# Kernel optimization log

Hardware: AMD Instinct MI355X
Metric: run time of the kernel (lower is better)

## Reference

```python
import jax, jax.numpy as jnp
import numpy as np

B, T, C, H = 4, 2048, 1024, 16
D = C // H  # head_dim = 64


def setup_inputs() -> dict:
    key = jax.random.key(0)
    ks = jax.random.split(key, 4)
    scale = 1.0 / np.sqrt(C)
    return {
        "x": jax.random.normal(ks[0], (B, T, C), dtype=jnp.float32),
        "attn_mask": jnp.ones((B, T), dtype=jnp.int32),
        "W_qkv": jax.random.normal(ks[1], (C, 3 * C), dtype=jnp.float32) * scale,
        "b_qkv": jnp.zeros((3 * C,), dtype=jnp.float32),
        "W_proj": jax.random.normal(ks[2], (C, C), dtype=jnp.float32) * scale,
        "b_proj": jnp.zeros((C,), dtype=jnp.float32),
    }


def reference(x, attn_mask, W_qkv, b_qkv, W_proj, b_proj):
    b, t, c = x.shape
    qkv = x @ W_qkv + b_qkv                      # (B,T,3C)
    q, k, v = jnp.split(qkv, 3, axis=-1)
    # b t (h d) -> b h t d
    q = q.reshape(b, t, H, D).transpose(0, 2, 1, 3)
    k = k.reshape(b, t, H, D).transpose(0, 2, 1, 3)
    v = v.reshape(b, t, H, D).transpose(0, 2, 1, 3)
    att = jnp.einsum("bhtd,bhsd->bhts", q, k) / jnp.sqrt(jnp.float32(D))
    causal = jnp.tril(jnp.ones((t, t), dtype=bool))[None, None]       # (1,1,T,T)
    pad = (attn_mask[:, None, None, :t] != 0)                         # (B,1,1,T)
    att = jnp.where(causal & pad, att, -jnp.inf)
    att = jax.nn.softmax(att, axis=-1)
    y = jnp.einsum("bhts,bhsd->bhtd", att, v)   # (B,H,T,D)
    y = y.transpose(0, 2, 1, 3).reshape(b, t, c)
    return y @ W_proj + b_proj
```

## Files before the change

### kernel.cpp

```cpp
#include <hip/hip_runtime.h>
#include <math.h>

#define B_ 4
#define T_ 2048
#define C_ 1024
#define H_ 16
#define D_ 64
#define M_ (B_*T_)
#define N1_ (3*C_)

typedef __attribute__((ext_vector_type(8))) short bf16x8;
typedef __attribute__((ext_vector_type(4))) short bf16x4;
typedef __attribute__((ext_vector_type(4))) float f32x4;
typedef __attribute__((ext_vector_type(16))) float f32x16;

__device__ __forceinline__ short f2bf(float f){
  union { float f; unsigned u; } v; v.f = f;
  unsigned r = (v.u + 0x7fffu + ((v.u >> 16) & 1u)) >> 16;
  return (short)r;
}

__device__ __forceinline__ unsigned cvtpk(float lo, float hi){
  unsigned r;
  asm("v_cvt_pk_bf16_f32 %0, %1, %2" : "=v"(r) : "v"(lo), "v"(hi));
  return r;
}

__device__ __forceinline__ void plswap(unsigned &a, unsigned &b){
  asm volatile("v_permlane32_swap_b32 %0, %1" : "+v"(a), "+v"(b));
}
__device__ __forceinline__ float xhalf_add(float x){
  unsigned a = __float_as_uint(x), b = a;
  asm volatile("v_permlane32_swap_b32 %0, %1" : "+v"(a), "+v"(b));
  return __uint_as_float(a) + __uint_as_float(b);
}

__device__ __forceinline__ void gll16(const void* g, void* l){
  __builtin_amdgcn_global_load_lds((const __attribute__((address_space(1))) void*)g,
                                   (__attribute__((address_space(3))) void*)l, 16, 0, 0);
}

__global__ __launch_bounds__(256) void convx(const float* __restrict__ x, short* __restrict__ xb, int n){
  int i = (blockIdx.x*256 + threadIdx.x)*8;
  if (i >= n) return;
  float4 a = *(const float4*)(x+i), b = *(const float4*)(x+i+4);
  bf16x8 o;
  o[0]=f2bf(a.x); o[1]=f2bf(a.y); o[2]=f2bf(a.z); o[3]=f2bf(a.w);
  o[4]=f2bf(b.x); o[5]=f2bf(b.y); o[6]=f2bf(b.z); o[7]=f2bf(b.w);
  *(bf16x8*)(xb+i) = o;
}

__global__ __launch_bounds__(256) void transw(const float* __restrict__ W, short* __restrict__ Wt, int K, int N){
  __shared__ float tl[64][72];
  int tid = threadIdx.x;
  int n0 = blockIdx.x*64, k0 = blockIdx.y*64;
  #pragma unroll
  for (int i=0;i<4;i++){
    int row = (tid>>4) + i*16;
    int col4 = (tid&15)*4;
    float4 v = *(const float4*)&W[(size_t)(k0+row)*N + n0 + col4];
    *(float4*)&tl[row][col4] = v;
  }
  __syncthreads();
  #pragma unroll
  for (int i=0;i<2;i++){
    int nr = (tid>>3) + i*32;
    int ch = tid&7;
    bf16x8 o;
    #pragma unroll
    for (int e=0;e<8;e++) o[e] = f2bf(tl[ch*8+e][nr]);
    *(bf16x8*)&Wt[(size_t)(n0+nr)*K + k0 + ch*8] = o;
  }
}

template<int OUTBF>
__global__ __launch_bounds__(256) void gemm_bt(const short* __restrict__ A, const short* __restrict__ Bt,
           const float* __restrict__ bias, short* __restrict__ outb, float* __restrict__ outf,
           int M, int N, int K)
{
  __shared__ short As[128*32];
  __shared__ short Bs[128*32];
  const int tid = threadIdx.x;
  const int wv = tid >> 6, ln = tid & 63;
  const int lnr = ln & 15, lg = ln >> 4;
  const int nx = gridDim.x;
  const int nwg = nx * gridDim.y;
  const int lin = blockIdx.x + nx * blockIdx.y;
  const int swz = (lin & 7) * (nwg >> 3) + (lin >> 3);
  const int m0 = (swz / nx) * 128, n0 = (swz % nx) * 128;
  const int wm = wv >> 1, wn = wv & 1;

  int aoff[4], boff[4];
  #pragma unroll
  for (int mi=0;mi<4;mi++){
    int row = wm*64 + mi*16 + lnr;
    aoff[mi] = row*64 + ((lg ^ ((row>>1)&3)) << 4);
  }
  #pragma unroll
  for (int ni=0;ni<4;ni++){
    int row = wn*64 + ni*16 + lnr;
    boff[ni] = row*64 + ((lg ^ ((row>>1)&3)) << 4);
  }

  f32x4 acc[4][4];
  #pragma unroll
  for(int i=0;i<4;i++)
    #pragma unroll
    for(int j=0;j<4;j++) acc[i][j] = (f32x4){0.f,0.f,0.f,0.f};

  for (int k0 = 0; k0 < K; k0 += 32){
    #pragma unroll
    for (int c = 0; c < 2; c++){
      int i = c*256 + tid;
      int r = i >> 2;
      int blk = (i&3) ^ ((r>>1)&3);
      gll16(A  + (size_t)(m0 + r)*K + k0 + blk*8, (void*)(As + (c*256 + wv*64)*8));
      gll16(Bt + (size_t)(n0 + r)*K + k0 + blk*8, (void*)(Bs + (c*256 + wv*64)*8));
    }
    __syncthreads();
    bf16x8 af[4], bfr[4];
    #pragma unroll
    for (int mi=0;mi<4;mi++) af[mi]  = *(const bf16x8*)((const char*)As + aoff[mi]);
    #pragma unroll
    for (int ni=0;ni<4;ni++) bfr[ni] = *(const bf16x8*)((const char*)Bs + boff[ni]);
    #pragma unroll
    for (int mi=0;mi<4;mi++)
      #pragma unroll
      for (int ni=0;ni<4;ni++)
        acc[mi][ni] = __builtin_amdgcn_mfma_f32_16x16x32_bf16(af[mi], bfr[ni], acc[mi][ni], 0,0,0);
    __syncthreads();
  }

  #pragma unroll
  for (int mi=0;mi<4;mi++){
    #pragma unroll
    for (int ni=0;ni<4;ni++){
      int col = n0 + wn*64 + ni*16 + lnr;
      float bv = bias[col];
      #pragma unroll
      for (int r=0;r<4;r++){
        int row = m0 + wm*64 + mi*16 + lg*4 + r;
        float v = acc[mi][ni][r] + bv;
        if (OUTBF) outb[(size_t)row*N + col] = f2bf(v);
        else       outf[(size_t)row*N + col] = v;
      }
    }
  }
}

__global__ __launch_bounds__(256) void transv(const short* __restrict__ qkv, short* __restrict__ vt){
  __shared__ short tl[64][72];
  int tid = threadIdx.x;
  int t0 = blockIdx.x*64, bh = blockIdx.y;
  int b = bh>>4, h = bh&15;
  int tr = tid>>2, cc = (tid&3)*16;
  const short* src = &qkv[(size_t)(b*T_ + t0 + tr)*N1_ + 2*C_ + h*D_ + cc];
  #pragma unroll
  for (int i=0;i<4;i++){
    bf16x4 v = *(const bf16x4*)(src + i*4);
    *(bf16x4*)&tl[tr][cc + i*4] = v;
  }
  __syncthreads();
  int d = tid>>2, tc = (tid&3)*16;
  #pragma unroll
  for (int i=0;i<2;i++){
    bf16x8 o;
    #pragma unroll
    for (int e=0;e<8;e++) o[e] = tl[tc + i*8 + e][d];
    *(bf16x8*)&vt[(size_t)(bh*D_ + d)*T_ + t0 + tc + i*8] = o;
  }
}

__global__ __launch_bounds__(256) void attn9(const short* __restrict__ qkv, const short* __restrict__ vt,
           const int* __restrict__ mask, short* __restrict__ yb)
{
  __shared__ short Ks[2][64*64];
  __shared__ short Vs[2][64*64];
  const int tid = threadIdx.x;
  const int wv = tid>>6, ln = tid&63;
  const int l31 = ln & 31, hi = ln >> 5;
  const int bh = blockIdx.x, b = bh>>4, hd = bh&15;
  const int c = 15 - (int)blockIdx.y;
  const float cexp = 0.18033688f;
  const float MC   = 11.541561f;

  const int srow = tid>>3;
  const int scol = (tid&7) ^ (srow&7);
  const short* kgb = qkv + (size_t)(b*T_ + srow)*N1_ + C_ + hd*D_ + scol*8;
  const short* vgb = vt  + (size_t)((bh<<6) + srow)*T_ + scol*8;
  int fa[4];
  #pragma unroll
  for (int i=0;i<4;i++)
    fa[i] = l31*128 + ((((i<<1)+hi) ^ (l31&7)) << 4);

  const int q0w = c*128 + wv*32;
  const int ntb  = 2*c + 2;
  const int myNt = 2*c + 1 + (wv>>1);

  bf16x8 qf[4];
  const short* qbase = qkv + (size_t)(b*T_ + q0w + l31)*N1_ + hd*D_ + hi*8;
  #pragma unroll
  for (int ds=0; ds<4; ds++) qf[ds] = *(const bf16x8*)(qbase + ds*16);

  f32x16 o0, o1;
  #pragma unroll
  for (int r=0;r<16;r++){ o0[r]=0.f; o1[r]=0.f; }
  float lsum = 0.f;

  int mv_next = mask[b*T_ + ln];
  {
    char* kd = (char*)Ks[0]; char* vd = (char*)Vs[0];
    gll16(kgb,                  kd + wv*1024);
    gll16(kgb + (size_t)32*N1_, kd + 4096 + wv*1024);
    gll16(vgb,                  vd + wv*1024);
    gll16(vgb + (size_t)32*T_,  vd + 4096 + wv*1024);
  }
  __syncthreads();

  #pragma unroll 1
  for (int jt = 0; jt < ntb; jt++){
    const int j0 = jt << 6;
    int mv_cur = mv_next;
    if (jt+1 < ntb){
      mv_next = mask[b*T_ + ((jt+1)<<6) + ln];
      char* kd = (char*)Ks[(jt+1)&1]; char* vd = (char*)Vs[(jt+1)&1];
      const short* kg = kgb + (size_t)((jt+1)<<6)*N1_;
      const short* vg = vgb + ((jt+1)<<6);
      gll16(kg,                  kd + wv*1024);
      gll16(kg + (size_t)32*N1_, kd + 4096 + wv*1024);
      gll16(vg,                  vd + wv*1024);
      gll16(vg + (size_t)32*T_,  vd + 4096 + wv*1024);
    }
    unsigned long long bm = __ballot(mv_cur != 0);

    if (jt < myNt){
      const char* ksb = (const char*)Ks[jt&1];
      const char* vsb = (const char*)Vs[jt&1];
      f32x16 s0, s1;
      #pragma unroll
      for (int r=0;r<16;r++){ s0[r]=0.f; s1[r]=0.f; }
      __builtin_amdgcn_s_setprio(1);
      #pragma unroll
      for (int ds=0; ds<4; ds++){
        bf16x8 k0 = *(const bf16x8*)(ksb + fa[ds]);
        bf16x8 k1 = *(const bf16x8*)(ksb + fa[ds] + 4096);
        s0 = __builtin_amdgcn_mfma_f32_32x32x16_bf16(k0, qf[ds], s0, 0,0,0);
        s1 = __builtin_amdgcn_mfma_f32_32x32x16_bf16(k1, qf[ds], s1, 0,0,0);
      }
      __builtin_amdgcn_s_setprio(0);

      const int qglob = q0w + l31;
      const bool allm = (bm == ~0ull);
      if (!allm){
        #pragma unroll
        for (int r=0;r<16;r++){
          int kr = (r&3) + 8*(r>>2) + 4*hi;
          bool ok0 = (j0 + kr      <= qglob) && ((bm >> kr) & 1);
          bool ok1 = (j0 + kr + 32 <= qglob) && ((bm >> (kr+32)) & 1);
          s0[r] = ok0 ? s0[r] : -INFINITY;
          s1[r] = ok1 ? s1[r] : -INFINITY;
        }
      } else if (j0 + 63 > q0w){
        #pragma unroll
        for (int r=0;r<16;r++){
          int kr = (r&3) + 8*(r>>2) + 4*hi;
          s0[r] = (j0 + kr      <= qglob) ? s0[r] : -INFINITY;
          s1[r] = (j0 + kr + 32 <= qglob) ? s1[r] : -INFINITY;
        }
      }

      #pragma unroll
      for (int r=0;r<16;r++){
        s0[r] = __builtin_amdgcn_exp2f(__builtin_fmaf(s0[r], cexp, -MC));
        s1[r] = __builtin_amdgcn_exp2f(__builtin_fmaf(s1[r], cexp, -MC));
      }
      float u[8];
      #pragma unroll
      for (int i=0;i<8;i++) u[i] = (s0[i]+s0[i+8]) + (s1[i]+s1[i+8]);
      #pragma unroll
      for (int i=0;i<4;i++) u[i] = u[i] + u[i+4];
      float ps = (u[0]+u[1]) + (u[2]+u[3]);
      lsum += xhalf_add(ps);

      unsigned LA[2][4], LB[2][4];
      #pragma unroll
      for (int rq=0; rq<4; rq++){
        LA[0][rq] = cvtpk(s0[4*rq],   s0[4*rq+1]);
        LB[0][rq] = cvtpk(s0[4*rq+2], s0[4*rq+3]);
        LA[1][rq] = cvtpk(s1[4*rq],   s1[4*rq+1]);
        LB[1][rq] = cvtpk(s1[4*rq+2], s1[4*rq+3]);
      }

      #pragma unroll
      for (int kt2=0; kt2<4; kt2++){
        const int kt = kt2>>1, sub = kt2&1;
        bf16x8 v0 = *(const bf16x8*)(vsb + fa[kt2]);
        bf16x8 v1 = *(const bf16x8*)(vsb + fa[kt2] + 4096);
        unsigned a0 = LA[kt][2*sub], a1 = LA[kt][2*sub+1];
        unsigned b0 = LB[kt][2*sub], b1 = LB[kt][2*sub+1];
        plswap(a0, a1);
        plswap(b0, b1);
        union { unsigned u[4]; bf16x8 v; } pf;
        pf.u[0] = a0; pf.u[1] = b0; pf.u[2] = a1; pf.u[3] = b1;
        __builtin_amdgcn_s_setprio(1);
        o0 = __builtin_amdgcn_mfma_f32_32x32x16_bf16(pf.v, v0, o0, 0,0,0);
        o1 = __builtin_amdgcn_mfma_f32_32x32x16_bf16(pf.v, v1, o1, 0,0,0);
        __builtin_amdgcn_s_setprio(0);
      }
    }
    __syncthreads();
  }

  float linv = 1.0f / lsum;
  #pragma unroll
  for (int r=0;r<16;r++){
    int qs = (r&3) + 8*(r>>2) + 4*hi;
    float lv = __shfl(linv, qs);
    size_t base = (size_t)(b*T_ + q0w + qs)*C_ + hd*D_ + l31;
    yb[base]      = f2bf(o0[r]*lv);
    yb[base + 32] = f2bf(o1[r]*lv);
  }
}

extern "C" void kernel_launch(void* const* d_in, const int* in_sizes, int n_in,
                              void* d_out, int out_size, void* d_ws, size_t ws_size,
                              hipStream_t stream){
  const float* x     = (const float*)d_in[0];
  const int*   mask  = (const int*)d_in[1];
  const float* Wqkv  = (const float*)d_in[2];
  const float* bqkv  = (const float*)d_in[3];
  const float* Wproj = (const float*)d_in[4];
  const float* bproj = (const float*)d_in[5];
  float* out = (float*)d_out;

  char* w = (char*)d_ws;
  short* xb     = (short*)w; w += (size_t)M_*C_*2;
  short* wqkvT  = (short*)w; w += (size_t)N1_*C_*2;
  short* wprojT = (short*)w; w += (size_t)C_*C_*2;
  short* qkvb   = (short*)w; w += (size_t)M_*N1_*2;
  short* vtb    = (short*)w; w += (size_t)B_*H_*D_*T_*2;
  short* yb     = (short*)w; w += (size_t)M_*C_*2;

  convx<<<dim3((M_*C_)/(256*8)), 256, 0, stream>>>(x, xb, M_*C_);
  transw<<<dim3(N1_/64, C_/64), 256, 0, stream>>>(Wqkv, wqkvT, C_, N1_);
  transw<<<dim3(C_/64,  C_/64), 256, 0, stream>>>(Wproj, wprojT, C_, C_);
  gemm_bt<1><<<dim3(N1_/128, M_/128), 256, 0, stream>>>(xb, wqkvT, bqkv, qkvb, nullptr, M_, N1_, C_);
  transv<<<dim3(T_/64, B_*H_), 256, 0, stream>>>(qkvb, vtb);
  attn9<<<dim3(B_*H_, 16), 256, 0, stream>>>(qkvb, vtb, mask, yb);
  gemm_bt<0><<<dim3(C_/128, M_/128), 256, 0, stream>>>(yb, wprojT, bproj, nullptr, out, M_, C_, C_);
}
```

Measured before the change: 188.9 us.

## Triple-buffer GEMM with 256x128 tiles, 512 threads and K=64 stages

Rewrites the bf16 GEMM kernel to use 256x128 output tiles per 512-thread block. K is consumed in 64-wide steps through a three-stage LDS ring buffer, using async global-to-LDS loads with explicit vmcnt waits and raw s_barrier instead of two __syncthreads per step. The intent is to overlap global loads with MFMA work and cut barrier and issue overhead, with setprio raised during the MFMA burst. It uses 144KB of LDS per block, which limits occupancy to one block per CU and halves the number of workgroups.

```diff
diff --git a/kernel.cpp b/kernel.cpp
--- a/kernel.cpp
+++ b/kernel.cpp
@@ -74,61 +74,96 @@
 }
 
 template<int OUTBF>
-__global__ __launch_bounds__(256) void gemm_bt(const short* __restrict__ A, const short* __restrict__ Bt,
+__global__ __launch_bounds__(512) void gemm_bt(const short* __restrict__ A, const short* __restrict__ Bt,
            const float* __restrict__ bias, short* __restrict__ outb, float* __restrict__ outf,
            int M, int N, int K)
 {
-  __shared__ short As[128*32];
-  __shared__ short Bs[128*32];
+  __shared__ __attribute__((aligned(128))) char LDSC[147456];
   const int tid = threadIdx.x;
-  const int wv = tid >> 6, ln = tid & 63;
-  const int lnr = ln & 15, lg = ln >> 4;
+  const int wv = tid>>6, ln = tid&63;
+  const int lnr = ln&15, lg = ln>>4;
+  const int wm = wv>>1, wn = wv&1;
   const int nx = gridDim.x;
-  const int nwg = nx * gridDim.y;
-  const int lin = blockIdx.x + nx * blockIdx.y;
-  const int swz = (lin & 7) * (nwg >> 3) + (lin >> 3);
-  const int m0 = (swz / nx) * 128, n0 = (swz % nx) * 128;
-  const int wm = wv >> 1, wn = wv & 1;
-
-  int aoff[4], boff[4];
-  #pragma unroll
-  for (int mi=0;mi<4;mi++){
-    int row = wm*64 + mi*16 + lnr;
-    aoff[mi] = row*64 + ((lg ^ ((row>>1)&3)) << 4);
-  }
-  #pragma unroll
-  for (int ni=0;ni<4;ni++){
-    int row = wn*64 + ni*16 + lnr;
-    boff[ni] = row*64 + ((lg ^ ((row>>1)&3)) << 4);
-  }
+  const int nwg = nx*gridDim.y;
+  const int lin = blockIdx.x + nx*blockIdx.y;
+  const int swz = (lin&7)*(nwg>>3) + (lin>>3);
+  const int m0 = (swz/nx)*256, n0 = (swz%nx)*128;
+
+  const int srA = tid>>3;
+  const int sg  = (tid&7) ^ (srA&7);
+  const short* Ag = A  + (size_t)(m0 + srA)*K + sg*8;
+  const short* Bg = Bt + (size_t)(n0 + srA)*K + sg*8;
+
+  const int fsw = (lg ^ (lnr&7))<<4;
+  const int aln = (wm*64 + lnr)*128 + fsw;
+  const int bln = (wn*64 + lnr)*128 + fsw;
+
+  auto STAGE = [&](int kt, int bi){
+    const short* a = Ag + kt*64;
+    const short* b = Bg + kt*64;
+    char* ab = LDSC + bi*32768 + wv*1024;
+    char* bb = LDSC + 98304 + bi*16384 + wv*1024;
+    gll16(a,                ab);
+    gll16(a + (size_t)64*K, ab + 8192);
+    gll16(a + (size_t)128*K, ab + 16384);
+    gll16(a + (size_t)192*K, ab + 24576);
+    gll16(b,                bb);
+    gll16(b + (size_t)64*K, bb + 8192);
+  };
 
   f32x4 acc[4][4];
   #pragma unroll
-  for(int i=0;i<4;i++)
-    #pragma unroll
-    for(int j=0;j<4;j++) acc[i][j] = (f32x4){0.f,0.f,0.f,0.f};
-
-  for (int k0 = 0; k0 < K; k0 += 32){
-    #pragma unroll
-    for (int c = 0; c < 2; c++){
-      int i = c*256 + tid;
-      int r = i >> 2;
-      int blk = (i&3) ^ ((r>>1)&3);
-      gll16(A  + (size_t)(m0 + r)*K + k0 + blk*8, (void*)(As + (c*256 + wv*64)*8));
-      gll16(Bt + (size_t)(n0 + r)*K + k0 + blk*8, (void*)(Bs + (c*256 + wv*64)*8));
+  for (int i=0;i<4;i++)
+    #pragma unroll
+    for (int j=0;j<4;j++) acc[i][j] = (f32x4){0.f,0.f,0.f,0.f};
+
+  const int NT = K >> 6;
+  STAGE(0, 0);
+  STAGE(1, 1);
+  asm volatile("s_waitcnt vmcnt(6)" ::: "memory");
+  __builtin_amdgcn_sched_barrier(0);
+  __builtin_amdgcn_s_barrier();
+  __builtin_amdgcn_sched_barrier(0);
+
+  int cb = 0, sb = 2;
+  #pragma unroll 1
+  for (int kt = 0; kt < NT; kt++){
+    if (kt + 2 < NT) STAGE(kt + 2, sb);
+
+    const char* ab = LDSC + cb*32768;
+    const char* bb = LDSC + 98304 + cb*16384;
+    bf16x8 af[4][2], bfr[4][2];
+    #pragma unroll
+    for (int mi=0;mi<4;mi++)
+      #pragma unroll
+      for (int ks=0;ks<2;ks++)
+        af[mi][ks] = *(const bf16x8*)(ab + ((aln + mi*2048) ^ (ks<<6)));
+    #pragma unroll
+    for (int ni=0;ni<4;ni++)
+      #pragma unroll
+      for (int ks=0;ks<2;ks++)
+        bfr[ni][ks] = *(const bf16x8*)(bb + ((bln + ni*2048) ^ (ks<<6)));
+
+    __builtin_amdgcn_s_setprio(1);
+    #pragma unroll
+    for (int mi=0;mi<4;mi++)
+      #pragma unroll
+      for (int ni=0;ni<4;ni++)
+        #pragma unroll
+        for (int ks=0;ks<2;ks++)
+          acc[mi][ni] = __builtin_amdgcn_mfma_f32_16x16x32_bf16(af[mi][ks], bfr[ni][ks], acc[mi][ni], 0,0,0);
+    __builtin_amdgcn_s_setprio(0);
+
+    if (kt < NT-1){
+      __builtin_amdgcn_sched_barrier(0);
+      if (kt < NT-2){ asm volatile("s_waitcnt vmcnt(6)" ::: "memory"); }
+      else          { asm volatile("s_waitcnt vmcnt(0)" ::: "memory"); }
+      __builtin_amdgcn_sched_barrier(0);
+      __builtin_amdgcn_s_barrier();
+      __builtin_amdgcn_sched_barrier(0);
     }
-    __syncthreads();
-    bf16x8 af[4], bfr[4];
-    #pragma unroll
-    for (int mi=0;mi<4;mi++) af[mi]  = *(const bf16x8*)((const char*)As + aoff[mi]);
-    #pragma unroll
-    for (int ni=0;ni<4;ni++) bfr[ni] = *(const bf16x8*)((const char*)Bs + boff[ni]);
-    #pragma unroll
-    for (int mi=0;mi<4;mi++)
-      #pragma unroll
-      for (int ni=0;ni<4;ni++)
-        acc[mi][ni] = __builtin_amdgcn_mfma_f32_16x16x32_bf16(af[mi], bfr[ni], acc[mi][ni], 0,0,0);
-    __syncthreads();
+    cb = (cb==2) ? 0 : cb+1;
+    sb = (sb==2) ? 0 : sb+1;
   }
 
   #pragma unroll
@@ -344,8 +379,8 @@
   convx<<<dim3((M_*C_)/(256*8)), 256, 0, stream>>>(x, xb, M_*C_);
   transw<<<dim3(N1_/64, C_/64), 256, 0, stream>>>(Wqkv, wqkvT, C_, N1_);
   transw<<<dim3(C_/64,  C_/64), 256, 0, stream>>>(Wproj, wprojT, C_, C_);
-  gemm_bt<1><<<dim3(N1_/128, M_/128), 256, 0, stream>>>(xb, wqkvT, bqkv, qkvb, nullptr, M_, N1_, C_);
+  gemm_bt<1><<<dim3(N1_/128, M_/256), 512, 0, stream>>>(xb, wqkvT, bqkv, qkvb, nullptr, M_, N1_, C_);
   transv<<<dim3(T_/64, B_*H_), 256, 0, stream>>>(qkvb, vtb);
   attn9<<<dim3(B_*H_, 16), 256, 0, stream>>>(qkvb, vtb, mask, yb);
-  gemm_bt<0><<<dim3(C_/128, M_/128), 256, 0, stream>>>(yb, wprojT, bproj, nullptr, out, M_, C_, C_);
-}
+  gemm_bt<0><<<dim3(C_/128, M_/256), 512, 0, stream>>>(yb, wprojT, bproj, nullptr, out, M_, C_, C_);
+}
```

After: 184.0 us. -2.6%, faster.
